# Kernel optimization log

Measured on AMD Instinct MI355X. Metric: run time of the kernel, lower is better.

Reference implementation:

```python
import jax, jax.numpy as jnp
import numpy as np

N = 40000      # nodes
E = 640000     # edges (avg degree 16)
H = 128        # hidden_dim
D = 4          # propagation_depth
G = 1250       # graphs in batch
T = 32         # target_dim
AF, AV = 9, 64   # atom categorical features, vocab per feature
BF, BV = 3, 8    # bond categorical features, vocab per feature


def silu(x):
    return x * jax.nn.sigmoid(x)


def setup_inputs() -> dict:
    key = jax.random.key(0)
    ks = jax.random.split(key, 32)
    s = 1.0 / np.sqrt(H)

    def w(i, shp, scale):
        return (jax.random.normal(ks[i], shp, jnp.float32) * scale).astype(jnp.float32)

    inp = {}
    inp["atom_feat"] = jax.random.randint(ks[0], (N, AF), 0, AV)
    inp["bond_feat"] = jax.random.randint(ks[1], (E, BF), 0, BV)
    inp["edge_src"] = jax.random.randint(ks[2], (E,), 0, N)
    inp["edge_dst"] = jax.random.randint(ks[3], (E,), 0, N)
    inp["node2graph"] = jnp.sort(jax.random.randint(ks[4], (N,), 0, G))

    inp["atom_emb"] = w(5, (AF, AV, H), 0.1)
    inp["bond_emb"] = w(6, (BF, BV, H), 0.1)
    # message MLP: Linear(3H,H)+SiLU, Linear(H,H)+SiLU (last_activation=mid_activation)
    inp["msg_W1"] = w(7, (D, 3 * H, H), 1.0 / np.sqrt(3 * H))
    inp["msg_b1"] = jnp.zeros((D, H), jnp.float32)
    inp["msg_W2"] = w(8, (D, H, H), s)
    inp["msg_b2"] = jnp.zeros((D, H), jnp.float32)
    # soft edge gate: Linear(H,1) + sigmoid
    inp["gate_W"] = w(9, (D, H, 1), s)
    inp["gate_b"] = jnp.zeros((D, 1), jnp.float32)
    # update MLP: Linear(H,H)+SiLU, Linear(H,H) (last None)
    inp["upd_W1"] = w(10, (D, H, H), s)
    inp["upd_b1"] = jnp.zeros((D, H), jnp.float32)
    inp["upd_W2"] = w(11, (D, H, H), s)
    inp["upd_b2"] = jnp.zeros((D, H), jnp.float32)
    # node_wise_output: Linear(H,H)+SiLU, Linear(H,H) (last None)
    inp["out_W1"] = w(12, (H, H), s)
    inp["out_b1"] = jnp.zeros((H,), jnp.float32)
    inp["out_W2"] = w(13, (H, H), s)
    inp["out_b2"] = jnp.zeros((H,), jnp.float32)
    # readout output MLP: Linear(3H,H)+ReLU, Linear(H,T) (last None)
    inp["ro_W1"] = w(14, (3 * H, H), 1.0 / np.sqrt(3 * H))
    inp["ro_b1"] = jnp.zeros((H,), jnp.float32)
    inp["ro_W2"] = w(15, (H, T), s)
    inp["ro_b2"] = jnp.zeros((T,), jnp.float32)
    return inp


def _forward(atom_feat, bond_feat, edge_src, edge_dst, node2graph,
             atom_emb, bond_emb,
             msg_W1, msg_b1, msg_W2, msg_b2, gate_W, gate_b,
             upd_W1, upd_b1, upd_W2, upd_b2,
             out_W1, out_b1, out_W2, out_b2,
             ro_W1, ro_b1, ro_W2, ro_b2):
    # Atom/Bond encoders: sum of per-feature categorical embeddings
    h = atom_emb[jnp.arange(AF), atom_feat].sum(axis=1)        # [N, H]
    e = bond_emb[jnp.arange(BF), bond_feat].sum(axis=1)        # [E, H]

    for l in range(D):
        src = h[edge_src]                                      # [E, H]
        dst = h[edge_dst]                                      # [E, H]
        m_in = jnp.concatenate([src, dst, e], axis=-1)         # [E, 3H]
        m = silu(silu(m_in @ msg_W1[l] + msg_b1[l]) @ msg_W2[l] + msg_b2[l])
        gate = jax.nn.sigmoid(m @ gate_W[l] + gate_b[l])       # [E, 1]
        m = m * gate
        m_sum = jax.ops.segment_sum(m, edge_dst, num_segments=N)  # [N, H]
        u_in = m_sum + h
        h_new = silu(u_in @ upd_W1[l] + upd_b1[l]) @ upd_W2[l] + upd_b2[l]
        h = h_new + h

    # node-wise output network
    h = silu(h @ out_W1 + out_b1) @ out_W2 + out_b2            # [N, H]

    # per-graph readouts: sum / mean / max
    sums = jax.ops.segment_sum(h, node2graph, num_segments=G)  # [G, H]
    cnt = jax.ops.segment_sum(jnp.ones((N, 1), h.dtype), node2graph, num_segments=G)
    mean = sums / jnp.maximum(cnt, 1.0)
    mx = jax.ops.segment_max(h, node2graph, num_segments=G)
    mx = jnp.where(cnt > 0, mx, 0.0)
    readout = jnp.concatenate([sums, mean, mx], axis=-1)       # [G, 3H]

    return jax.nn.relu(readout @ ro_W1 + ro_b1) @ ro_W2 + ro_b2  # [G, T]


def reference(atom_feat, bond_feat, edge_src, edge_dst, node2graph,
              atom_emb, bond_emb,
              msg_W1, msg_b1, msg_W2, msg_b2, gate_W, gate_b,
              upd_W1, upd_b1, upd_W2, upd_b2,
              out_W1, out_b1, out_W2, out_b2,
              ro_W1, ro_b1, ro_W2, ro_b2):
    return _forward(atom_feat, bond_feat, edge_src, edge_dst, node2graph,
                    atom_emb, bond_emb,
                    msg_W1, msg_b1, msg_W2, msg_b2, gate_W, gate_b,
                    upd_W1, upd_b1, upd_W2, upd_b2,
                    out_W1, out_b1, out_W2, out_b2,
                    ro_W1, ro_b1, ro_W2, ro_b2)
```

## Files before the change

kernel.cpp:

```cpp
#include <hip/hip_runtime.h>
#include <hip/hip_bf16.h>
#include <hip/hip_fp16.h>

#define NN 40000
#define NE 640000
#define HD 128
#define DEPTH 4
#define NG 1250
#define TD 32
#define AFN 9
#define AVN 64
#define BFN 3
#define BVN 8
#define NBLK2 (NE / 128)

typedef short bf16x8 __attribute__((ext_vector_type(8)));
typedef _Float16 f16x8 __attribute__((ext_vector_type(8)));
typedef _Float16 f16x2 __attribute__((ext_vector_type(2)));
typedef float f32x4 __attribute__((ext_vector_type(4)));

__device__ __forceinline__ uint cvtpk(float lo, float hi){
  uint r; asm("v_cvt_pk_bf16_f32 %0, %1, %2" : "=v"(r) : "v"(lo), "v"(hi)); return r;
}
__device__ __forceinline__ ushort f2bf(float x){ return (ushort)cvtpk(x, x); }
__device__ __forceinline__ float rcpfa(float x){ return __builtin_amdgcn_rcpf(x); }
__device__ __forceinline__ float siluf(float x){ return x * rcpfa(1.f + __expf(-x)); }
__device__ __forceinline__ float sigmf(float x){ return rcpfa(1.f + __expf(-x)); }
__device__ __forceinline__ uint packbf2(float a, float b){ return cvtpk(a, b); }

__device__ __forceinline__ __half2 silu_h2(__half2 x){
  const __half2 nl2e = __float2half2_rn(-1.44269504f);
  const __half2 one  = __float2half2_rn(1.f);
  __half2 e = h2exp2(__hmul2(x, nl2e));
  return __hmul2(x, h2rcp(__hadd2(one, e)));
}
union H2U { __half2 h; f16x2 v; uint u; };
__device__ __forceinline__ __half2 pkrtz(float lo, float hi){
  auto t = __builtin_amdgcn_cvt_pkrtz(lo, hi);
  H2U r; __builtin_memcpy(&r.u, &t, 4); return r.h;
}

__device__ __forceinline__ void pack_one(const float* __restrict__ src,
                                         ushort* __restrict__ dst,
                                         int K, int L, int isf16){
  int total = L * K * HD;
  for (int idx = blockIdx.x * blockDim.x + threadIdx.x; idx < total;
       idx += gridDim.x * blockDim.x){
    int l = idx / (K * HD);
    int r = idx - l * K * HD;
    int k = r / HD;
    int n = r - k * HD;
    float v = src[idx];
    ushort o;
    if (isf16){ __half hv = __float2half_rn(v); o = *(ushort*)&hv; }
    else o = f2bf(v);
    dst[(size_t)l * K * HD + ((size_t)(k >> 3) * HD + n) * 8 + (k & 7)] = o;
  }
}
__global__ void pack6(const float* s0, const float* s1, const float* s2,
                      const float* s3, const float* s4, const float* s5,
                      ushort* d0, ushort* d1, ushort* d2,
                      ushort* d3, ushort* d4, ushort* d5){
  switch (blockIdx.y){
    case 0: pack_one(s0, d0, 384, DEPTH, 0); break;
    case 1: pack_one(s1, d1, HD, DEPTH, 1); break;
    case 2: pack_one(s2, d2, HD, DEPTH, 0); break;
    case 3: pack_one(s3, d3, HD, DEPTH, 0); break;
    case 4: pack_one(s4, d4, HD, 1, 0); break;
    default: pack_one(s5, d5, HD, 1, 0); break;
  }
}

__global__ void zero_i(int* __restrict__ p, int n){
  for (int i = blockIdx.x * blockDim.x + threadIdx.x; i < n; i += gridDim.x * blockDim.x)
    p[i] = 0;
}

__global__ void atom_encode(const int* __restrict__ feat, const float* __restrict__ emb,
                            float* __restrict__ h, ushort* __restrict__ hbf){
  int n = blockIdx.x;
  int c = threadIdx.x;
  float acc = 0.f;
#pragma unroll
  for (int f = 0; f < AFN; ++f){
    int v = feat[n * AFN + f];
    acc += emb[(size_t)(f * AVN + v) * HD + c];
  }
  h[(size_t)n * HD + c] = acc;
  hbf[(size_t)n * HD + c] = f2bf(acc);
}

__global__ void ebf_k(const float* __restrict__ bemb, ushort* __restrict__ ebf){
  const int cid = blockIdx.x;
  const int c = threadIdx.x;
  const int f0 = cid >> 6, f1 = (cid >> 3) & 7, f2 = cid & 7;
  float v = bemb[(size_t)(0 * BVN + f0) * HD + c]
          + bemb[(size_t)(1 * BVN + f1) * HD + c]
          + bemb[(size_t)(2 * BVN + f2) * HD + c];
  ebf[(size_t)cid * HD + c] = f2bf(v);
}

__global__ void hist_k(const int* __restrict__ edst, int* __restrict__ deg){
  for (int e = blockIdx.x * blockDim.x + threadIdx.x; e < NE; e += gridDim.x * blockDim.x)
    atomicAdd(&deg[edst[e]], 1);
}

__global__ __launch_bounds__(1024) void scan_head(const int* __restrict__ deg,
                                                  int* __restrict__ head){
  __shared__ int buf[1024];
  const int t = threadIdx.x;
  const int base = t * 40;
  int s = 0;
  int dloc[40];
  if (t < 1000){
#pragma unroll
    for (int i = 0; i < 40; ++i){ dloc[i] = deg[base + i]; s += dloc[i]; }
  }
  buf[t] = s;
  __syncthreads();
  for (int ofs = 1; ofs < 1024; ofs <<= 1){
    int x = (t >= ofs) ? buf[t - ofs] : 0;
    __syncthreads();
    buf[t] += x;
    __syncthreads();
  }
  if (t < 1000){
    int run = buf[t] - s;
#pragma unroll
    for (int i = 0; i < 40; ++i){ head[base + i] = run; run += dloc[i]; }
  }
}

__global__ void scatter_k(const int* __restrict__ esrc, const int* __restrict__ edst,
                          const int* __restrict__ bfeat, int* __restrict__ head,
                          int* __restrict__ esrc_p, int* __restrict__ dst_p,
                          int* __restrict__ cid_p){
  for (int e = blockIdx.x * blockDim.x + threadIdx.x; e < NE; e += gridDim.x * blockDim.x){
    const int d = edst[e];
    const int pos = atomicAdd(&head[d], 1);
    esrc_p[pos] = esrc[e];
    dst_p[pos] = d;
    cid_p[pos] = bfeat[e * 3 + 0] * 64 + bfeat[e * 3 + 1] * 8 + bfeat[e * 3 + 2];
  }
}

__global__ __launch_bounds__(256) void pre_k(
    const ushort* __restrict__ hbf, const ushort* __restrict__ W1p,
    __half* __restrict__ prea, __half* __restrict__ preb,
    uint* __restrict__ msum2)
{
  const int tid = threadIdx.x;
  const int n0 = blockIdx.x * 64;
  {
    uint4* mz = (uint4*)(msum2 + (size_t)n0 * 64);
    const uint4 z = make_uint4(0u, 0u, 0u, 0u);
#pragma unroll
    for (int i = 0; i < 4; ++i) mz[tid + i * 256] = z;
  }
  const int lane = tid & 63, wv = tid >> 6;
  const int lr = lane & 15, lg = lane >> 4;
  const int arow = n0 + wv * 16 + lr;
  bf16x8 a[4];
#pragma unroll
  for (int ks = 0; ks < 4; ++ks)
    a[ks] = *(const bf16x8*)(hbf + (size_t)arow * HD + ks * 32 + lg * 8);
  const f32x4 zero = {0.f, 0.f, 0.f, 0.f};
  f32x4 acc[16];
#pragma unroll
  for (int i = 0; i < 16; ++i) acc[i] = zero;
#pragma unroll
  for (int ks = 0; ks < 4; ++ks){
#pragma unroll
    for (int ct = 0; ct < 16; ++ct){
      const int oct = ks * 4 + lg + ((ct >= 8) ? 16 : 0);
      const int ncol = (ct & 7) * 16 + lr;
      bf16x8 b = *(const bf16x8*)(W1p + ((size_t)oct * HD + ncol) * 8);
      acc[ct] = __builtin_amdgcn_mfma_f32_16x16x32_bf16(a[ks], b, acc[ct], 0, 0, 0);
    }
  }
#pragma unroll
  for (int ct = 0; ct < 16; ++ct){
    __half* dstp = (ct < 8) ? prea : preb;
    const int ncol = (ct & 7) * 16 + lr;
#pragma unroll
    for (int r = 0; r < 4; ++r){
      const int nrow = n0 + wv * 16 + lg * 4 + r;
      dstp[(size_t)nrow * HD + ncol] = __float2half_rn(acc[ct][r]);
    }
  }
}

__global__ __launch_bounds__(256) void ew1c_k(
    const ushort* __restrict__ ebf, const ushort* __restrict__ W1p_all,
    const float* __restrict__ b1_all, __half* __restrict__ ecb_all)
{
  const int l = blockIdx.y;
  const ushort* W1p = W1p_all + (size_t)l * 384 * HD;
  const float* b1v = b1_all + l * HD;
  __half* ecb = ecb_all + (size_t)l * 512 * HD;
  const int tid = threadIdx.x;
  const int c0 = blockIdx.x * 64;
  const int lane = tid & 63, wv = tid >> 6;
  const int lr = lane & 15, lg = lane >> 4;
  const int arow = c0 + wv * 16 + lr;
  bf16x8 a[4];
#pragma unroll
  for (int ks = 0; ks < 4; ++ks)
    a[ks] = *(const bf16x8*)(ebf + (size_t)arow * HD + ks * 32 + lg * 8);
  const f32x4 zero = {0.f, 0.f, 0.f, 0.f};
  f32x4 acc[8];
#pragma unroll
  for (int i = 0; i < 8; ++i) acc[i] = zero;
#pragma unroll
  for (int ks = 0; ks < 4; ++ks){
#pragma unroll
    for (int ct = 0; ct < 8; ++ct){
      const int oct = ks * 4 + lg + 32;
      const int ncol = ct * 16 + lr;
      bf16x8 b = *(const bf16x8*)(W1p + ((size_t)oct * HD + ncol) * 8);
      acc[ct] = __builtin_amdgcn_mfma_f32_16x16x32_bf16(a[ks], b, acc[ct], 0, 0, 0);
    }
  }
#pragma unroll
  for (int ct = 0; ct < 8; ++ct){
    const int ncol = ct * 16 + lr;
    const float bias = b1v[ncol];
#pragma unroll
    for (int r = 0; r < 4; ++r){
      const int nrow = c0 + wv * 16 + lg * 4 + r;
      ecb[(size_t)nrow * HD + ncol] = __float2half_rn(acc[ct][r] + bias);
    }
  }
}

__device__ __forceinline__ void build_af(
    const __half* __restrict__ prea, const __half* __restrict__ preb,
    const __half* __restrict__ ecb, int s, int d, int c, int lg, f16x8* af)
{
#pragma unroll
  for (int ks = 0; ks < 4; ++ks){
    const int off = ks * 32 + lg * 8;
    union { uint4 q; __half2 h[4]; f16x8 v; } ua, ub, uc, uo;
    ua.q = *(const uint4*)(prea + (size_t)s * HD + off);
    ub.q = *(const uint4*)(preb + (size_t)d * HD + off);
    uc.q = *(const uint4*)(ecb + (size_t)c * HD + off);
#pragma unroll
    for (int j = 0; j < 4; ++j)
      uo.h[j] = silu_h2(__hadd2(__hadd2(ua.h[j], ub.h[j]), uc.h[j]));
    af[ks] = uo.v;
  }
}

__device__ __forceinline__ void edge_epilogue(
    f32x4* acc, int lr, int lg, int rowbase,
    const float* b2l, const float* b2h, const __half2* gwh, float gbias,
    uint* Ms)
{
  __half2 mh[4][4];
#pragma unroll
  for (int ct = 0; ct < 4; ++ct){
#pragma unroll
    for (int r = 0; r < 4; ++r)
      mh[ct][r] = silu_h2(pkrtz(acc[ct][r] + b2l[ct], acc[ct + 4][r] + b2h[ct]));
  }
#pragma unroll
  for (int r = 0; r < 4; ++r){
    float sgs = 0.f;
#pragma unroll
    for (int ct = 0; ct < 4; ++ct){
      H2U a, b; a.h = mh[ct][r]; b.h = gwh[ct];
      sgs = __builtin_amdgcn_fdot2(a.v, b.v, sgs, false);
    }
    sgs += __shfl_xor(sgs, 1); sgs += __shfl_xor(sgs, 2);
    sgs += __shfl_xor(sgs, 4); sgs += __shfl_xor(sgs, 8);
    const __half2 gh = __float2half2_rn(sigmf(sgs + gbias));
#pragma unroll
    for (int ct = 0; ct < 4; ++ct) mh[ct][r] = __hmul2(mh[ct][r], gh);
  }
#pragma unroll
  for (int ct = 0; ct < 4; ++ct){
    const int ui = ct * 16 + lr;
#pragma unroll
    for (int r = 0; r < 4; ++r){
      const int lrow = rowbase + lg * 4 + r;
      H2U w; w.h = mh[ct][r];
      *(uint*)((char*)Ms + lrow * 256 + (((uint)(ui * 4)) ^ ((uint)((lrow & 7) << 4)))) = w.u;
    }
  }
}

__global__ __launch_bounds__(256, 4) void msg2_kernel(
    const __half* __restrict__ prea, const __half* __restrict__ preb,
    const __half* __restrict__ ecb,
    const int* __restrict__ esrc_p, const int* __restrict__ dst_p,
    const int* __restrict__ cid_p,
    const __half* __restrict__ W2p, const float* __restrict__ b2v,
    const float* __restrict__ gw, const float* __restrict__ gb,
    __half2* __restrict__ msum2)
{
  __shared__ uint Ms[128 * 64];
  __shared__ int dsh[128];
  const int tid = threadIdx.x;
  const int bid = (int)blockIdx.x;
  const int bsw = (bid & 7) * (NBLK2 >> 3) + (bid >> 3);
  const int e0 = bsw * 128;
  if (tid < 128) dsh[tid] = dst_p[e0 + tid];

  const int lane = tid & 63;
  const int wv = tid >> 6;
  const int lr = lane & 15, lg = lane >> 4;
  const int row0 = e0 + wv * 16 + lr;
  const int row1 = row0 + 64;
  const int s0 = esrc_p[row0], d0 = dst_p[row0], c0 = cid_p[row0];
  const int s1 = esrc_p[row1], d1 = dst_p[row1], c1 = cid_p[row1];

  f16x8 af0[4], af1[4];
  build_af(prea, preb, ecb, s0, d0, c0, lg, af0);
  build_af(prea, preb, ecb, s1, d1, c1, lg, af1);

  const f32x4 zero = {0.f, 0.f, 0.f, 0.f};
  f32x4 acc0[8], acc1[8];
#pragma unroll
  for (int i = 0; i < 8; ++i){ acc0[i] = zero; acc1[i] = zero; }
#pragma unroll
  for (int ks = 0; ks < 4; ++ks){
    const __half* wb = W2p + ((size_t)(ks * 4 + lg) * HD + lr) * 8;
#pragma unroll
    for (int ct = 0; ct < 8; ++ct){
      f16x8 b = *(const f16x8*)(wb + ct * 16 * 8);
      acc0[ct] = __builtin_amdgcn_mfma_f32_16x16x32_f16(af0[ks], b, acc0[ct], 0, 0, 0);
      acc1[ct] = __builtin_amdgcn_mfma_f32_16x16x32_f16(af1[ks], b, acc1[ct], 0, 0, 0);
    }
  }

  float b2l[4], b2h[4];
  __half2 gwh[4];
#pragma unroll
  for (int ct = 0; ct < 4; ++ct){
    b2l[ct] = b2v[ct * 16 + lr];
    b2h[ct] = b2v[ct * 16 + lr + 64];
    gwh[ct] = pkrtz(gw[ct * 16 + lr], gw[ct * 16 + lr + 64]);
  }
  const float gbias = gb[0];
  edge_epilogue(acc0, lr, lg, wv * 16, b2l, b2h, gwh, gbias, Ms);
  edge_epilogue(acc1, lr, lg, 64 + wv * 16, b2l, b2h, gwh, gbias, Ms);
  __syncthreads();

  {
    const int cp = tid & 63;
    const int seg = tid >> 6;
    const int r0 = seg * 32, r1 = r0 + 32;
    float rl = 0.f, rh = 0.f;
    int cur = dsh[r0];
    for (int r = r0; r < r1; ++r){
      const int dd = dsh[r];
      if (dd != cur){
        unsafeAtomicAdd(&msum2[(size_t)cur * 64 + cp], pkrtz(rl, rh));
        rl = 0.f; rh = 0.f; cur = dd;
      }
      H2U w;
      w.u = *(const uint*)((const char*)Ms + r * 256 +
                           (((uint)(cp * 4)) ^ ((uint)((r & 7) << 4))));
      rl += __low2float(w.h); rh += __high2float(w.h);
    }
    unsafeAtomicAdd(&msum2[(size_t)cur * 64 + cp], pkrtz(rl, rh));
  }
}

template <int MODE>
__global__ __launch_bounds__(256) void node_mlp(
    const float* hin, const uint* __restrict__ msum2,
    const ushort* __restrict__ W1p, const ushort* __restrict__ W2p,
    const float* __restrict__ b1v, const float* __restrict__ b2v,
    float* outp, ushort* __restrict__ hbf)
{
  __shared__ ushort At[64 * 128];
  __shared__ ushort Tt[64 * 128];
  const int tid = threadIdx.x;
  const int n0 = blockIdx.x * 64;

  {
    const int nl = tid >> 2, part = tid & 3;
    const int node = n0 + nl;
    const float4* hp = (const float4*)(hin + (size_t)node * HD + part * 32);
    const uint* mp = (MODE == 0) ? (msum2 + (size_t)node * 64) : nullptr;
    const bool hiHalf = (MODE == 0) && (part >= 2);
    char* rowp = (char*)At + nl * 256;
    const uint sw = (uint)((nl & 7) << 4);
#pragma unroll
    for (int j = 0; j < 4; ++j){
      float4 x0 = hp[j * 2 + 0], x1 = hp[j * 2 + 1];
      if (MODE == 0){
        const int cp0 = (part & 1) * 32 + j * 8;
        uint4 ma = *(const uint4*)(mp + cp0);
        uint4 mb = *(const uint4*)(mp + cp0 + 4);
        H2U w0, w1, w2, w3, w4, w5, w6, w7;
        w0.u = ma.x; w1.u = ma.y; w2.u = ma.z; w3.u = ma.w;
        w4.u = mb.x; w5.u = mb.y; w6.u = mb.z; w7.u = mb.w;
        if (hiHalf){
          x0.x += __high2float(w0.h); x0.y += __high2float(w1.h);
          x0.z += __high2float(w2.h); x0.w += __high2float(w3.h);
          x1.x += __high2float(w4.h); x1.y += __high2float(w5.h);
          x1.z += __high2float(w6.h); x1.w += __high2float(w7.h);
        } else {
          x0.x += __low2float(w0.h); x0.y += __low2float(w1.h);
          x0.z += __low2float(w2.h); x0.w += __low2float(w3.h);
          x1.x += __low2float(w4.h); x1.y += __low2float(w5.h);
          x1.z += __low2float(w6.h); x1.w += __low2float(w7.h);
        }
      }
      uint4 o;
      o.x = packbf2(x0.x, x0.y); o.y = packbf2(x0.z, x0.w);
      o.z = packbf2(x1.x, x1.y); o.w = packbf2(x1.z, x1.w);
      uint cb = (uint)(part * 64 + j * 16);
      *(uint4*)(rowp + (cb ^ sw)) = o;
    }
  }
  __syncthreads();

  const int lane = tid & 63;
  const int wv = tid >> 6;
  const int lr = lane & 15, lg = lane >> 4;
  const int rowbase = wv * 16;
  const f32x4 zero = {0.f, 0.f, 0.f, 0.f};
  const int arow = rowbase + lr;
  const char* arp = (const char*)At + arow * 256;
  const uint asw = (uint)((arow & 7) << 4);

  f32x4 acc[8];
#pragma unroll
  for (int i = 0; i < 8; ++i) acc[i] = zero;
#pragma unroll
  for (int ks = 0; ks < 4; ++ks){
    uint cb = (uint)(ks * 64 + lg * 16);
    bf16x8 a = *(const bf16x8*)(arp + (cb ^ asw));
    const ushort* wbase = W1p + ((size_t)(ks * 4 + lg) * 128 + lr) * 8;
#pragma unroll
    for (int ct = 0; ct < 8; ++ct){
      bf16x8 b = *(const bf16x8*)(wbase + ct * 16 * 8);
      acc[ct] = __builtin_amdgcn_mfma_f32_16x16x32_bf16(a, b, acc[ct], 0, 0, 0);
    }
  }
#pragma unroll
  for (int ct = 0; ct < 8; ++ct){
    const int col = ct * 16 + lr;
    const float bias = b1v[col];
#pragma unroll
    for (int r = 0; r < 4; ++r){
      const int row = rowbase + lg * 4 + r;
      float v = siluf(acc[ct][r] + bias);
      *(ushort*)((char*)Tt + row * 256 + (((uint)(col * 2)) ^ ((uint)(row & 7) << 4))) = f2bf(v);
    }
  }
  __syncthreads();

  f32x4 acc2[8];
#pragma unroll
  for (int i = 0; i < 8; ++i) acc2[i] = zero;
  {
    const char* trp = (const char*)Tt + arow * 256;
#pragma unroll
    for (int ks = 0; ks < 4; ++ks){
      uint cb = (uint)(ks * 64 + lg * 16);
      bf16x8 a = *(const bf16x8*)(trp + (cb ^ asw));
      const ushort* wbase = W2p + ((size_t)(ks * 4 + lg) * 128 + lr) * 8;
#pragma unroll
      for (int ct = 0; ct < 8; ++ct){
        bf16x8 b = *(const bf16x8*)(wbase + ct * 16 * 8);
        acc2[ct] = __builtin_amdgcn_mfma_f32_16x16x32_bf16(a, b, acc2[ct], 0, 0, 0);
      }
    }
  }
#pragma unroll
  for (int ct = 0; ct < 8; ++ct){
    const int col = ct * 16 + lr;
    const float bias = b2v[col];
#pragma unroll
    for (int r = 0; r < 4; ++r){
      const int node = n0 + rowbase + lg * 4 + r;
      float v = acc2[ct][r] + bias;
      if (MODE == 0) v += hin[(size_t)node * HD + col];
      outp[(size_t)node * HD + col] = v;
      if (MODE == 0) hbf[(size_t)node * HD + col] = f2bf(v);
    }
  }
}

__global__ __launch_bounds__(128) void readout_final(
    const float* __restrict__ hout, const int* __restrict__ n2g,
    const float* __restrict__ W1, const float* __restrict__ b1,
    const float* __restrict__ W2, const float* __restrict__ b2,
    float* __restrict__ out){
  __shared__ float rsh[384];
  __shared__ float hr[128];
  const int g = blockIdx.x;
  const int c = threadIdx.x;
  int lo, hi;
  { int a = 0, b = NN; while (a < b){ int mid = (a + b) >> 1; if (n2g[mid] < g) a = mid + 1; else b = mid; } lo = a; }
  { int a = lo, b = NN; while (a < b){ int mid = (a + b) >> 1; if (n2g[mid] < g + 1) a = mid + 1; else b = mid; } hi = a; }
  float s = 0.f, mx = -3.4e38f;
  for (int n = lo; n < hi; ++n){
    float v = hout[(size_t)n * HD + c];
    s += v; mx = fmaxf(mx, v);
  }
  const int cnt = hi - lo;
  float mean = (cnt > 0) ? s / (float)cnt : 0.f;
  if (cnt == 0){ s = 0.f; mx = 0.f; }
  rsh[c] = s; rsh[128 + c] = mean; rsh[256 + c] = mx;
  __syncthreads();
  float acc = b1[c];
#pragma unroll 4
  for (int j = 0; j < 384; ++j) acc += rsh[j] * W1[j * 128 + c];
  hr[c] = fmaxf(acc, 0.f);
  __syncthreads();
  if (c < TD){
    float o = b2[c];
#pragma unroll 4
    for (int j = 0; j < 128; ++j) o += hr[j] * W2[j * TD + c];
    out[(size_t)g * TD + c] = o;
  }
}

extern "C" void kernel_launch(void* const* d_in, const int* in_sizes, int n_in,
                              void* d_out, int out_size, void* d_ws, size_t ws_size,
                              hipStream_t stream)
{
  const int*   atom_feat  = (const int*)  d_in[0];
  const int*   bond_feat  = (const int*)  d_in[1];
  const int*   edge_src   = (const int*)  d_in[2];
  const int*   edge_dst   = (const int*)  d_in[3];
  const int*   node2graph = (const int*)  d_in[4];
  const float* atom_emb   = (const float*)d_in[5];
  const float* bond_emb   = (const float*)d_in[6];
  const float* msg_W1     = (const float*)d_in[7];
  const float* msg_b1     = (const float*)d_in[8];
  const float* msg_W2     = (const float*)d_in[9];
  const float* msg_b2     = (const float*)d_in[10];
  const float* gate_W     = (const float*)d_in[11];
  const float* gate_b     = (const float*)d_in[12];
  const float* upd_W1     = (const float*)d_in[13];
  const float* upd_b1     = (const float*)d_in[14];
  const float* upd_W2     = (const float*)d_in[15];
  const float* upd_b2     = (const float*)d_in[16];
  const float* out_W1     = (const float*)d_in[17];
  const float* out_b1     = (const float*)d_in[18];
  const float* out_W2     = (const float*)d_in[19];
  const float* out_b2     = (const float*)d_in[20];
  const float* ro_W1      = (const float*)d_in[21];
  const float* ro_b1      = (const float*)d_in[22];
  const float* ro_W2      = (const float*)d_in[23];
  const float* ro_b2      = (const float*)d_in[24];
  (void)in_sizes; (void)n_in; (void)out_size; (void)ws_size;

  char* ws = (char*)d_ws;
  size_t off = 0;
  auto alloc = [&](size_t bytes) -> char* {
    char* p = ws + off;
    off = (off + bytes + 255) & ~(size_t)255;
    return p;
  };
  float*   h      = (float*)  alloc((size_t)NN * HD * 4);
  float*   hout   = (float*)  alloc((size_t)NN * HD * 4);
  ushort*  hbf    = (ushort*) alloc((size_t)NN * HD * 2);
  __half2* msum2  = (__half2*)alloc((size_t)NN * 64 * 4);
  ushort*  msgW1p = (ushort*) alloc((size_t)DEPTH * 384 * HD * 2);
  ushort*  msgW2p = (ushort*) alloc((size_t)DEPTH * HD * HD * 2);
  ushort*  updW1p = (ushort*) alloc((size_t)DEPTH * HD * HD * 2);
  ushort*  updW2p = (ushort*) alloc((size_t)DEPTH * HD * HD * 2);
  ushort*  outW1p = (ushort*) alloc((size_t)HD * HD * 2);
  ushort*  outW2p = (ushort*) alloc((size_t)HD * HD * 2);
  ushort*  ebf    = (ushort*) alloc((size_t)512 * HD * 2);
  __half*  ecb    = (__half*) alloc((size_t)DEPTH * 512 * HD * 2);
  __half*  prea   = (__half*) alloc((size_t)NN * HD * 2);
  __half*  preb   = (__half*) alloc((size_t)NN * HD * 2);
  int*     deg    = (int*)    alloc((size_t)NN * 4);
  int*     head   = (int*)    alloc((size_t)NN * 4);
  int*     esrc_p = (int*)    alloc((size_t)NE * 4);
  int*     dst_p  = (int*)    alloc((size_t)NE * 4);
  int*     cid_p  = (int*)    alloc((size_t)NE * 4);

  pack6<<<dim3(48, 6), 256, 0, stream>>>(msg_W1, msg_W2, upd_W1, upd_W2, out_W1, out_W2,
                                         msgW1p, msgW2p, updW1p, updW2p, outW1p, outW2p);
  atom_encode<<<NN, HD, 0, stream>>>(atom_feat, atom_emb, h, hbf);
  ebf_k<<<512, HD, 0, stream>>>(bond_emb, ebf);
  ew1c_k<<<dim3(8, DEPTH), 256, 0, stream>>>(ebf, msgW1p, msg_b1, ecb);

  zero_i<<<160, 256, 0, stream>>>(deg, NN);
  hist_k<<<640, 256, 0, stream>>>(edge_dst, deg);
  scan_head<<<1, 1024, 0, stream>>>(deg, head);
  scatter_k<<<640, 256, 0, stream>>>(edge_src, edge_dst, bond_feat, head,
                                     esrc_p, dst_p, cid_p);

  for (int l = 0; l < DEPTH; ++l){
    pre_k<<<NN / 64, 256, 0, stream>>>(hbf, msgW1p + (size_t)l * 384 * HD, prea, preb,
                                       (uint*)msum2);
    msg2_kernel<<<NBLK2, 256, 0, stream>>>(
        prea, preb, ecb + (size_t)l * 512 * HD,
        esrc_p, dst_p, cid_p,
        (const __half*)msgW2p + (size_t)l * HD * HD,
        msg_b2 + l * HD, gate_W + l * HD, gate_b + l, msum2);
    node_mlp<0><<<NN / 64, 256, 0, stream>>>(
        h, (const uint*)msum2,
        updW1p + (size_t)l * HD * HD, updW2p + (size_t)l * HD * HD,
        upd_b1 + l * HD, upd_b2 + l * HD, h, hbf);
  }
  node_mlp<1><<<NN / 64, 256, 0, stream>>>(
      h, nullptr, outW1p, outW2p, out_b1, out_b2, hout, nullptr);
  readout_final<<<NG, 128, 0, stream>>>(hout, node2graph, ro_W1, ro_b1, ro_W2, ro_b2,
                                        (float*)d_out);
}
```

Before: 695.4 us.

## Scatter edge messages directly from registers instead of staging in LDS

```diff
diff --git a/kernel.cpp b/kernel.cpp
--- a/kernel.cpp
+++ b/kernel.cpp
@@ -251,10 +251,11 @@
   }
 }
 
-__device__ __forceinline__ void edge_epilogue(
-    f32x4* acc, int lr, int lg, int rowbase,
+__device__ __forceinline__ void edge_finish(
+    const f32x4* acc, int lr, int lg, int e0, int rowbase,
+    const int* __restrict__ dst_p,
     const float* b2l, const float* b2h, const __half2* gwh, float gbias,
-    uint* Ms)
+    __half2* __restrict__ msum2)
 {
   __half2 mh[4][4];
 #pragma unroll
@@ -277,15 +278,26 @@
 #pragma unroll
     for (int ct = 0; ct < 4; ++ct) mh[ct][r] = __hmul2(mh[ct][r], gh);
   }
+  const int rb = e0 + rowbase + lg * 4;
+  int dl[4];
+#pragma unroll
+  for (int r = 0; r < 4; ++r) dl[r] = dst_p[rb + r];
 #pragma unroll
   for (int ct = 0; ct < 4; ++ct){
-    const int ui = ct * 16 + lr;
-#pragma unroll
-    for (int r = 0; r < 4; ++r){
-      const int lrow = rowbase + lg * 4 + r;
-      H2U w; w.h = mh[ct][r];
-      *(uint*)((char*)Ms + lrow * 256 + (((uint)(ui * 4)) ^ ((uint)((lrow & 7) << 4)))) = w.u;
-    }
+    const int cp = ct * 16 + lr;
+    float rl = __low2float(mh[ct][0]), rh = __high2float(mh[ct][0]);
+    int cur = dl[0];
+#pragma unroll
+    for (int r = 1; r < 4; ++r){
+      if (dl[r] == cur){
+        rl += __low2float(mh[ct][r]); rh += __high2float(mh[ct][r]);
+      } else {
+        unsafeAtomicAdd(&msum2[(size_t)cur * 64 + cp], pkrtz(rl, rh));
+        rl = __low2float(mh[ct][r]); rh = __high2float(mh[ct][r]);
+        cur = dl[r];
+      }
+    }
+    unsafeAtomicAdd(&msum2[(size_t)cur * 64 + cp], pkrtz(rl, rh));
   }
 }
 
@@ -298,13 +310,10 @@
     const float* __restrict__ gw, const float* __restrict__ gb,
     __half2* __restrict__ msum2)
 {
-  __shared__ uint Ms[128 * 64];
-  __shared__ int dsh[128];
   const int tid = threadIdx.x;
   const int bid = (int)blockIdx.x;
   const int bsw = (bid & 7) * (NBLK2 >> 3) + (bid >> 3);
   const int e0 = bsw * 128;
-  if (tid < 128) dsh[tid] = dst_p[e0 + tid];
 
   const int lane = tid & 63;
   const int wv = tid >> 6;
@@ -342,29 +351,8 @@
     gwh[ct] = pkrtz(gw[ct * 16 + lr], gw[ct * 16 + lr + 64]);
   }
   const float gbias = gb[0];
-  edge_epilogue(acc0, lr, lg, wv * 16, b2l, b2h, gwh, gbias, Ms);
-  edge_epilogue(acc1, lr, lg, 64 + wv * 16, b2l, b2h, gwh, gbias, Ms);
-  __syncthreads();
-
-  {
-    const int cp = tid & 63;
-    const int seg = tid >> 6;
-    const int r0 = seg * 32, r1 = r0 + 32;
-    float rl = 0.f, rh = 0.f;
-    int cur = dsh[r0];
-    for (int r = r0; r < r1; ++r){
-      const int dd = dsh[r];
-      if (dd != cur){
-        unsafeAtomicAdd(&msum2[(size_t)cur * 64 + cp], pkrtz(rl, rh));
-        rl = 0.f; rh = 0.f; cur = dd;
-      }
-      H2U w;
-      w.u = *(const uint*)((const char*)Ms + r * 256 +
-                           (((uint)(cp * 4)) ^ ((uint)((r & 7) << 4))));
-      rl += __low2float(w.h); rh += __high2float(w.h);
-    }
-    unsafeAtomicAdd(&msum2[(size_t)cur * 64 + cp], pkrtz(rl, rh));
-  }
+  edge_finish(acc0, lr, lg, e0, wv * 16, dst_p, b2l, b2h, gwh, gbias, msum2);
+  edge_finish(acc1, lr, lg, e0, 64 + wv * 16, dst_p, b2l, b2h, gwh, gbias, msum2);
 }
 
 template <int MODE>
```

New measurement: 907.8 us. +30.5%, slower.
